# Performance work log

Hardware: AMD Instinct MI355X
Metric: run time of the kernel (lower is better)

Reference implementation:

```python
import jax, jax.numpy as jnp
import numpy as np

B, S, D = 2, 2048, 1024
NUM_HEADS = 16
HEAD_DIM = D // NUM_HEADS


def setup_inputs() -> dict:
    key = jax.random.key(0)
    k1, k2, k3, k4 = jax.random.split(key, 4)
    # Weights stored as [d_in, d_out] so projection is x @ W (torch Linear weight transposed).
    scale = 1.0 / np.sqrt(D)
    return {
        "x": jax.random.normal(k1, (B, S, D), dtype=jnp.float32),
        "W_q": jax.random.normal(k2, (D, D), dtype=jnp.float32) * scale,
        "W_k": jax.random.normal(k3, (D, D), dtype=jnp.float32) * scale,
        "W_v": jax.random.normal(k4, (D, D), dtype=jnp.float32) * scale,
    }


def reference(x, W_q, W_k, W_v):
    b, s, d = x.shape
    hd = d // NUM_HEADS
    # QKV projections (no bias, qkv_bias=False)
    q = (x @ W_q).reshape(b, s, NUM_HEADS, hd).transpose(0, 2, 1, 3)  # [B,H,S,hd]
    k = (x @ W_k).reshape(b, s, NUM_HEADS, hd).transpose(0, 2, 1, 3)
    v = (x @ W_v).reshape(b, s, NUM_HEADS, hd).transpose(0, 2, 1, 3)
    # Scaled scores with causal masking (strict upper triangle masked)
    scores = jnp.einsum("bhqd,bhkd->bhqk", q, k) / jnp.sqrt(jnp.float32(hd))
    causal = jnp.triu(jnp.ones((s, s), dtype=bool), 1)  # True = masked
    scores = jnp.where(causal, -jnp.inf, scores)
    attn = jax.nn.softmax(scores, axis=-1)  # dropout is identity (drop_rate=0.0)
    out = jnp.einsum("bhqk,bhkd->bqhd", attn, v).reshape(b, s, d)
    return out
```

## Files before the change

### kernel.cpp

```cpp
#include <hip/hip_runtime.h>


typedef unsigned short u16;
typedef unsigned long long u64;
typedef __bf16 bf16x8 __attribute__((ext_vector_type(8)));
typedef float f32x4 __attribute__((ext_vector_type(4)));
typedef u16 u16x8 __attribute__((ext_vector_type(8)));

#define NB 2
#define NS 2048
#define ND 1024
#define NH 16
#define HD 64

__device__ __forceinline__ u16 f2bf(float f) {
    unsigned int u = __float_as_uint(f);
    unsigned int r = u + 0x7fffu + ((u >> 16) & 1u);
    return (u16)(r >> 16);
}

__device__ __forceinline__ f32x4 mfma16(bf16x8 a, bf16x8 b, f32x4 c) {
    return __builtin_amdgcn_mfma_f32_16x16x32_bf16(a, b, c, 0, 0, 0);
}

__device__ __forceinline__ void gl_lds16(const void* g, void* l) {
    __builtin_amdgcn_global_load_lds(
        (const __attribute__((address_space(1))) unsigned int*)g,
        (__attribute__((address_space(3))) unsigned int*)l, 16, 0, 0);
}

__device__ __forceinline__ bf16x8 ldsw(const u16* base, int row, int colb) {
    return *(const bf16x8*)((const char*)base + row * 128 +
                            (colb ^ ((row & 7) << 4)));
}

__global__ __launch_bounds__(256) void convx_k(const float* __restrict__ x,
                                               u16* __restrict__ xb) {
    int i = (blockIdx.x * 256 + threadIdx.x) * 8;
    const float4* p = (const float4*)(x + i);
    float4 a = p[0], c = p[1];
    u16x8 r;
    r[0] = f2bf(a.x); r[1] = f2bf(a.y); r[2] = f2bf(a.z); r[3] = f2bf(a.w);
    r[4] = f2bf(c.x); r[5] = f2bf(c.y); r[6] = f2bf(c.z); r[7] = f2bf(c.w);
    *(u16x8*)(xb + i) = r;
}

__global__ __launch_bounds__(256) void convw_k(const float* __restrict__ wq,
                                               const float* __restrict__ wk,
                                               const float* __restrict__ wv,
                                               u16* __restrict__ wt) {
    __shared__ float tile[32][33];
    const int z = blockIdx.z;
    const float* W = (z == 0) ? wq : (z == 1) ? wk : wv;
    const int k0 = blockIdx.x * 32, n0 = blockIdx.y * 32;
    const int tx = threadIdx.x & 31, ty = threadIdx.x >> 5;
#pragma unroll
    for (int rr = 0; rr < 32; rr += 8)
        tile[ty + rr][tx] = W[(size_t)(k0 + ty + rr) * ND + n0 + tx];
    __syncthreads();
    u16* dst = wt + (size_t)z * ND * ND;
#pragma unroll
    for (int rr = 0; rr < 32; rr += 8)
        dst[(size_t)(n0 + ty + rr) * ND + k0 + tx] = f2bf(tile[tx][ty + rr]);
}

__global__ __launch_bounds__(256) void qkv_gemm_k(const u16* __restrict__ xb,
                                                  const u16* __restrict__ wt,
                                                  u16* __restrict__ qh,
                                                  u16* __restrict__ kh,
                                                  u16* __restrict__ vt) {
    __shared__ u16 At[128 * 64];
    __shared__ u16 Bt[3][64 * 64];
    const int m0 = blockIdx.x * 128;
    const int n0 = blockIdx.y * 64;
    const int t = threadIdx.x;
    const int lane = t & 63;
    const int wv = t >> 6;
    const int wm = (wv >> 1) * 64, wn = (wv & 1) * 32;
    const int fr = lane & 15;
    const int ks = lane >> 4;

    f32x4 acc[3][4][2] = {};

    for (int kt = 0; kt < ND; kt += 64) {
#pragma unroll
        for (int c = 0; c < 4; c++) {
            const int L = c * 4096 + t * 16;
            const int row = L >> 7;
            const int cb = (L & 127) ^ ((row & 7) << 4);
            gl_lds16((const char*)xb + (size_t)(m0 + row) * 2048 + kt * 2 + cb,
                     (char*)At + L);
        }
#pragma unroll
        for (int z = 0; z < 3; z++)
#pragma unroll
            for (int c = 0; c < 2; c++) {
                const int L = c * 4096 + t * 16;
                const int row = L >> 7;
                const int cb = (L & 127) ^ ((row & 7) << 4);
                gl_lds16((const char*)wt + (size_t)z * (ND * ND * 2) +
                             (size_t)(n0 + row) * 2048 + kt * 2 + cb,
                         (char*)&Bt[z][0] + L);
            }
        __syncthreads();

        bf16x8 fa[4][2];
#pragma unroll
        for (int i = 0; i < 4; i++)
#pragma unroll
            for (int c = 0; c < 2; c++)
                fa[i][c] = ldsw(At, wm + i * 16 + fr, c * 64 + ks * 16);

#pragma unroll
        for (int z = 0; z < 3; z++) {
            bf16x8 fb[2][2];
#pragma unroll
            for (int j = 0; j < 2; j++)
#pragma unroll
                for (int c = 0; c < 2; c++)
                    fb[j][c] =
                        ldsw(&Bt[z][0], wn + j * 16 + fr, c * 64 + ks * 16);
            if (z < 2) {
#pragma unroll
                for (int i = 0; i < 4; i++)
#pragma unroll
                    for (int j = 0; j < 2; j++)
#pragma unroll
                        for (int c = 0; c < 2; c++)
                            acc[z][i][j] =
                                mfma16(fa[i][c], fb[j][c], acc[z][i][j]);
            } else {
#pragma unroll
                for (int i = 0; i < 4; i++)
#pragma unroll
                    for (int j = 0; j < 2; j++)
#pragma unroll
                        for (int c = 0; c < 2; c++)
                            acc[z][i][j] =
                                mfma16(fb[j][c], fa[i][c], acc[z][i][j]);
            }
        }
        __syncthreads();
    }

#pragma unroll
    for (int z = 0; z < 2; z++) {
        u16* dst = (z == 0) ? qh : kh;
#pragma unroll
        for (int i = 0; i < 4; i++)
#pragma unroll
            for (int j = 0; j < 2; j++)
#pragma unroll
                for (int r = 0; r < 4; r++) {
                    int mg = m0 + wm + i * 16 + ks * 4 + r;
                    int ng = n0 + wn + j * 16 + fr;
                    int b = mg >> 11, s = mg & 2047;
                    int hh = ng >> 6, dd = ng & 63;
                    dst[(((size_t)b * NH + hh) * NS + s) * HD + dd] =
                        f2bf(acc[z][i][j][r]);
                }
    }
#pragma unroll
    for (int i = 0; i < 4; i++)
#pragma unroll
        for (int j = 0; j < 2; j++)
#pragma unroll
            for (int r = 0; r < 4; r++) {
                int ng = n0 + wn + j * 16 + ks * 4 + r;
                int mg = m0 + wm + i * 16 + fr;
                int b = mg >> 11, s = mg & 2047;
                int hh = ng >> 6, dd = ng & 63;
                int w = s & 63;
                int sp = (s & ~63) | (w & 32) | (((w >> 2) & 3) << 3) |
                         (((w >> 4) & 1) << 2) | (w & 3);
                vt[(((size_t)b * NH + hh) * HD + dd) * NS + sp] =
                    f2bf(acc[2][i][j][r]);
            }
}


__device__ __forceinline__ void stage_kv(const u16* __restrict__ K,
                                         const u16* __restrict__ V, int kv0,
                                         u16* Kl, u16* Vl, int t) {
#pragma unroll
    for (int c = 0; c < 2; c++) {
        const int L = c * 4096 + t * 16;
        const int row = L >> 7;
        const int cb = (L & 127) ^ ((row & 7) << 4);
        gl_lds16((const char*)K + (size_t)(kv0 + row) * 128 + cb,
                 (char*)Kl + L);
        gl_lds16((const char*)V + (size_t)row * (NS * 2) + kv0 * 2 + cb,
                 (char*)Vl + L);
    }
}

template <bool MASKED>
__device__ __forceinline__ void sm_pack(const f32x4* sc, bf16x8 pa[2],
                                        int kv0, int q0, int fr, int ks) {
    const int qg = q0 + fr;
#pragma unroll
    for (int kf = 0; kf < 4; kf++)
#pragma unroll
        for (int r = 0; r < 4; r++) {
            float s = sc[kf][r];
            if (MASKED && (kv0 + kf * 16 + ks * 4 + r > qg)) s = -3.0e38f;
            pa[kf >> 1][(kf & 1) * 4 + r] =
                (__bf16)exp2f(fmaf(s, 0.18033688f, -11.5415603f));
        }
}

__device__ __forceinline__ void pv_reg(const bf16x8 (*fv)[2],
                                       const bf16x8 pa[2], f32x4* o,
                                       f32x4& lacc, bf16x8 ones) {
    __builtin_amdgcn_s_setprio(1);
    lacc = mfma16(pa[0], ones, lacc);
    lacc = mfma16(pa[1], ones, lacc);
#pragma unroll
    for (int j = 0; j < 4; j++)
#pragma unroll
        for (int s2 = 0; s2 < 2; s2++) o[j] = mfma16(pa[s2], fv[j][s2], o[j]);
    __builtin_amdgcn_s_setprio(0);
}

__global__ __launch_bounds__(256, 2) void attn_k(const u16* __restrict__ qh,
                                                 const u16* __restrict__ kh,
                                                 const u16* __restrict__ vt,
                                                 float* __restrict__ out) {
    const int t = threadIdx.x, lane = t & 63, wv = t >> 6;
    const int fr = lane & 15, ks = lane >> 4;
    const int bh = blockIdx.x & 31;
    const int p = blockIdx.x >> 5;
    const int b = bh >> 4, h = bh & 15;
    const int tileA = 31 - p, tileB = p;
    const int qA = tileA * 64 + wv * 16;
    const int qB = tileB * 64 + wv * 16;
    const int nA = tileA + 1, nB = tileB + 1;
    const u16* Q = qh + (size_t)bh * NS * HD;
    const u16* K = kh + (size_t)bh * NS * HD;
    const u16* V = vt + (size_t)bh * HD * NS;

    __shared__ u16 Kl[2][64 * 64];
    __shared__ u16 Vl[2][64 * 64];

    bf16x8 fqA[2], fqB[2];
#pragma unroll
    for (int sl = 0; sl < 2; sl++) {
        fqA[sl] = *(const bf16x8*)&Q[(qA + fr) * HD + sl * 32 + ks * 8];
        fqB[sl] = *(const bf16x8*)&Q[(qB + fr) * HD + sl * 32 + ks * 8];
    }

    u16x8 ob;
#pragma unroll
    for (int j = 0; j < 8; j++) ob[j] = 0x3F80;
    const bf16x8 ones = __builtin_bit_cast(bf16x8, ob);

    f32x4 oA[4] = {}, oB[4] = {};
    f32x4 lA = {}, lB = {};

    stage_kv(K, V, 0, &Kl[0][0], &Vl[0][0], t);
    __syncthreads();

    for (int it = 0; it < nA; ++it) {
        const int cur = it & 1;
        const int kv0 = it * 64;
        if (it + 1 < nA)
            stage_kv(K, V, kv0 + 64, &Kl[cur ^ 1][0], &Vl[cur ^ 1][0], t);

        bf16x8 fk[4][2];
#pragma unroll
        for (int kf = 0; kf < 4; kf++)
#pragma unroll
            for (int sl = 0; sl < 2; sl++)
                fk[kf][sl] =
                    ldsw(&Kl[cur][0], kf * 16 + fr, sl * 64 + ks * 16);

        f32x4 scA[4] = {}, scB[4] = {};
        const bool doB = it < nB;
        __builtin_amdgcn_s_setprio(1);
#pragma unroll
        for (int kf = 0; kf < 4; kf++) {
            scA[kf] = mfma16(fk[kf][0], fqA[0], scA[kf]);
            scA[kf] = mfma16(fk[kf][1], fqA[1], scA[kf]);
        }
        if (doB) {
#pragma unroll
            for (int kf = 0; kf < 4; kf++) {
                scB[kf] = mfma16(fk[kf][0], fqB[0], scB[kf]);
                scB[kf] = mfma16(fk[kf][1], fqB[1], scB[kf]);
            }
        }
        __builtin_amdgcn_s_setprio(0);

        bf16x8 fv[4][2];
#pragma unroll
        for (int j = 0; j < 4; j++)
#pragma unroll
            for (int s2 = 0; s2 < 2; s2++)
                fv[j][s2] =
                    ldsw(&Vl[cur][0], j * 16 + fr, s2 * 64 + ks * 16);

        bf16x8 paA[2], paB[2];
        if (it == nA - 1)
            sm_pack<true>(scA, paA, kv0, qA, fr, ks);
        else
            sm_pack<false>(scA, paA, kv0, qA, fr, ks);
        pv_reg(fv, paA, oA, lA, ones);

        if (doB) {
            if (it == nB - 1)
                sm_pack<true>(scB, paB, kv0, qB, fr, ks);
            else
                sm_pack<false>(scB, paB, kv0, qB, fr, ks);
            pv_reg(fv, paB, oB, lB, ones);
        }

        __syncthreads();
    }

    float rlA[4], rlB[4];
#pragma unroll
    for (int r = 0; r < 4; r++) {
        rlA[r] = 1.0f / lA[r];
        rlB[r] = 1.0f / lB[r];
    }
#pragma unroll
    for (int j = 0; j < 4; j++)
#pragma unroll
        for (int r = 0; r < 4; r++) {
            const int qgA = qA + ks * 4 + r;
            const int qgB = qB + ks * 4 + r;
            out[((size_t)b * NS + qgA) * ND + h * HD + j * 16 + fr] =
                oA[j][r] * rlA[r];
            out[((size_t)b * NS + qgB) * ND + h * HD + j * 16 + fr] =
                oB[j][r] * rlB[r];
        }
}

extern "C" void kernel_launch(void* const* d_in, const int* in_sizes, int n_in,
                              void* d_out, int out_size, void* d_ws,
                              size_t ws_size, hipStream_t stream) {
    const float* x = (const float*)d_in[0];
    const float* wq = (const float*)d_in[1];
    const float* wk = (const float*)d_in[2];
    const float* wvp = (const float*)d_in[3];
    float* out = (float*)d_out;

    char* w8 = (char*)d_ws;
    u16* xb = (u16*)(w8);
    u16* wt = (u16*)(w8 + ((size_t)8 << 20));
    u16* qh = (u16*)(w8 + ((size_t)14 << 20));
    u16* kh = (u16*)(w8 + ((size_t)22 << 20));
    u16* vt = (u16*)(w8 + ((size_t)30 << 20));

    convx_k<<<(NB * NS * ND) / (256 * 8), 256, 0, stream>>>(x, xb);
    convw_k<<<dim3(ND / 32, ND / 32, 3), 256, 0, stream>>>(wq, wk, wvp, wt);
    qkv_gemm_k<<<dim3((NB * NS) / 128, ND / 64), 256, 0, stream>>>(
        xb, wt, qh, kh, vt);
    attn_k<<<512, 256, 0, stream>>>(qh, kh, vt, out);
}
```

Baseline: 81.67 us.

## Split paired causal query tiles into one tile per block

The attention kernel previously paired a long and a short causal query tile in each block so every block had equal work and shared its K/V loads. Now each block handles a single 64-row query tile, launching 1024 blocks ordered longest-first, and the launch bound's minimum-blocks hint is dropped. This halves per-block register state and raises parallelism. In exchange, K/V tiles are staged separately for each query tile rather than shared across the pair, and blocks now have unequal amounts of work.

```diff
diff --git a/kernel.cpp b/kernel.cpp
--- a/kernel.cpp
+++ b/kernel.cpp
@@ -222,19 +222,17 @@
     __builtin_amdgcn_s_setprio(0);
 }
 
-__global__ __launch_bounds__(256, 2) void attn_k(const u16* __restrict__ qh,
-                                                 const u16* __restrict__ kh,
-                                                 const u16* __restrict__ vt,
-                                                 float* __restrict__ out) {
+__global__ __launch_bounds__(256) void attn_k(const u16* __restrict__ qh,
+                                              const u16* __restrict__ kh,
+                                              const u16* __restrict__ vt,
+                                              float* __restrict__ out) {
     const int t = threadIdx.x, lane = t & 63, wv = t >> 6;
     const int fr = lane & 15, ks = lane >> 4;
     const int bh = blockIdx.x & 31;
-    const int p = blockIdx.x >> 5;
+    const int tile = 31 - (int)(blockIdx.x >> 5);
     const int b = bh >> 4, h = bh & 15;
-    const int tileA = 31 - p, tileB = p;
-    const int qA = tileA * 64 + wv * 16;
-    const int qB = tileB * 64 + wv * 16;
-    const int nA = tileA + 1, nB = tileB + 1;
+    const int q0 = tile * 64 + wv * 16;
+    const int nIt = tile + 1;
     const u16* Q = qh + (size_t)bh * NS * HD;
     const u16* K = kh + (size_t)bh * NS * HD;
     const u16* V = vt + (size_t)bh * HD * NS;
@@ -242,28 +240,26 @@
     __shared__ u16 Kl[2][64 * 64];
     __shared__ u16 Vl[2][64 * 64];
 
-    bf16x8 fqA[2], fqB[2];
-#pragma unroll
-    for (int sl = 0; sl < 2; sl++) {
-        fqA[sl] = *(const bf16x8*)&Q[(qA + fr) * HD + sl * 32 + ks * 8];
-        fqB[sl] = *(const bf16x8*)&Q[(qB + fr) * HD + sl * 32 + ks * 8];
-    }
+    bf16x8 fq[2];
+#pragma unroll
+    for (int sl = 0; sl < 2; sl++)
+        fq[sl] = *(const bf16x8*)&Q[(q0 + fr) * HD + sl * 32 + ks * 8];
 
     u16x8 ob;
 #pragma unroll
     for (int j = 0; j < 8; j++) ob[j] = 0x3F80;
     const bf16x8 ones = __builtin_bit_cast(bf16x8, ob);
 
-    f32x4 oA[4] = {}, oB[4] = {};
-    f32x4 lA = {}, lB = {};
+    f32x4 o[4] = {};
+    f32x4 l = {};
 
     stage_kv(K, V, 0, &Kl[0][0], &Vl[0][0], t);
     __syncthreads();
 
-    for (int it = 0; it < nA; ++it) {
+    for (int it = 0; it < nIt; ++it) {
         const int cur = it & 1;
         const int kv0 = it * 64;
-        if (it + 1 < nA)
+        if (it + 1 < nIt)
             stage_kv(K, V, kv0 + 64, &Kl[cur ^ 1][0], &Vl[cur ^ 1][0], t);
 
         bf16x8 fk[4][2];
@@ -274,20 +270,12 @@
                 fk[kf][sl] =
                     ldsw(&Kl[cur][0], kf * 16 + fr, sl * 64 + ks * 16);
 
-        f32x4 scA[4] = {}, scB[4] = {};
-        const bool doB = it < nB;
+        f32x4 sc[4] = {};
         __builtin_amdgcn_s_setprio(1);
 #pragma unroll
         for (int kf = 0; kf < 4; kf++) {
-            scA[kf] = mfma16(fk[kf][0], fqA[0], scA[kf]);
-            scA[kf] = mfma16(fk[kf][1], fqA[1], scA[kf]);
-        }
-        if (doB) {
-#pragma unroll
-            for (int kf = 0; kf < 4; kf++) {
-                scB[kf] = mfma16(fk[kf][0], fqB[0], scB[kf]);
-                scB[kf] = mfma16(fk[kf][1], fqB[1], scB[kf]);
-            }
+            sc[kf] = mfma16(fk[kf][0], fq[0], sc[kf]);
+            sc[kf] = mfma16(fk[kf][1], fq[1], sc[kf]);
         }
         __builtin_amdgcn_s_setprio(0);
 
@@ -299,40 +287,26 @@
                 fv[j][s2] =
                     ldsw(&Vl[cur][0], j * 16 + fr, s2 * 64 + ks * 16);
 
-        bf16x8 paA[2], paB[2];
-        if (it == nA - 1)
-            sm_pack<true>(scA, paA, kv0, qA, fr, ks);
+        bf16x8 pa[2];
+        if (it == nIt - 1)
+            sm_pack<true>(sc, pa, kv0, q0, fr, ks);
         else
-            sm_pack<false>(scA, paA, kv0, qA, fr, ks);
-        pv_reg(fv, paA, oA, lA, ones);
-
-        if (doB) {
-            if (it == nB - 1)
-                sm_pack<true>(scB, paB, kv0, qB, fr, ks);
-            else
-                sm_pack<false>(scB, paB, kv0, qB, fr, ks);
-            pv_reg(fv, paB, oB, lB, ones);
-        }
+            sm_pack<false>(sc, pa, kv0, q0, fr, ks);
+        pv_reg(fv, pa, o, l, ones);
 
         __syncthreads();
     }
 
-    float rlA[4], rlB[4];
-#pragma unroll
-    for (int r = 0; r < 4; r++) {
-        rlA[r] = 1.0f / lA[r];
-        rlB[r] = 1.0f / lB[r];
-    }
+    float rl[4];
+#pragma unroll
+    for (int r = 0; r < 4; r++) rl[r] = 1.0f / l[r];
 #pragma unroll
     for (int j = 0; j < 4; j++)
 #pragma unroll
         for (int r = 0; r < 4; r++) {
-            const int qgA = qA + ks * 4 + r;
-            const int qgB = qB + ks * 4 + r;
-            out[((size_t)b * NS + qgA) * ND + h * HD + j * 16 + fr] =
-                oA[j][r] * rlA[r];
-            out[((size_t)b * NS + qgB) * ND + h * HD + j * 16 + fr] =
-                oB[j][r] * rlB[r];
+            const int qg = q0 + ks * 4 + r;
+            out[((size_t)b * NS + qg) * ND + h * HD + j * 16 + fr] =
+                o[j][r] * rl[r];
         }
 }
 
@@ -356,5 +330,5 @@
     convw_k<<<dim3(ND / 32, ND / 32, 3), 256, 0, stream>>>(wq, wk, wvp, wt);
     qkv_gemm_k<<<dim3((NB * NS) / 128, ND / 64), 256, 0, stream>>>(
         xb, wt, qh, kh, vt);
-    attn_k<<<512, 256, 0, stream>>>(qh, kh, vt, out);
-}
+    attn_k<<<1024, 256, 0, stream>>>(qh, kh, vt, out);
+}
```

Measured after the change: 82.59 us. Within noise of the previous version (+1.1%).
